# Optimization experiments

Hardware: AMD Instinct MI355X
Metric: run time of the kernel (lower is better)

## Reference

```python
import jax, jax.numpy as jnp
import numpy as np

LSTM_SIZE = 64
NUM_OPS = 5
NUM_LAYERS = 7  # 2 warmup anchors + 5 sampled layers (layer_id 2..6)


def _lstm_cell(x, h, c, w_ih, w_hh, b_ih, b_hh):
    # torch LSTMCell gate order: i, f, g, o
    g = x @ w_ih.T + b_ih + h @ w_hh.T + b_hh  # [1, 4*64]
    i, f, gg, o = jnp.split(g, 4, axis=1)
    c2 = jax.nn.sigmoid(f) * c + jax.nn.sigmoid(i) * jnp.tanh(gg)
    h2 = jax.nn.sigmoid(o) * jnp.tanh(c2)
    return h2, c2


def _sampler(embed, w_ih, w_hh, b_ih, b_hh, w_soft, b_soft, b_soft_no_learn,
             w_attn1, w_attn2, v_attn, prev_c, prev_h, use_bias, key):
    keys = jax.random.split(key, 20)  # 5 layers * (2 index + 2 op) samples
    k = 0
    anchors, anchors_w1, arc_seq = [], [], []
    log_prob = jnp.float32(0.0)
    entropy = jnp.float32(0.0)
    inputs = embed[0][None, :]
    # warmup: two anchor slots (anchors are zeros, per original code)
    for _ in range(2):
        prev_h, prev_c = _lstm_cell(inputs, prev_h, prev_c, w_ih, w_hh, b_ih, b_hh)
        anchors.append(jnp.zeros((1, LSTM_SIZE), jnp.float32))
        anchors_w1.append(prev_h @ w_attn1.T)
    for layer_id in range(2, NUM_LAYERS):
        idxs, ops = [], []
        # sample 2 previous-layer indices via tiny attention
        for _ in range(2):
            prev_h, prev_c = _lstm_cell(inputs, prev_h, prev_c, w_ih, w_hh, b_ih, b_hh)
            query = jnp.concatenate(anchors_w1, axis=0)            # [layer_id, 64]
            q = jnp.tanh(query + prev_h @ w_attn2.T)               # broadcast [layer_id, 64]
            logits = (q @ v_attn.T).reshape(layer_id)              # [layer_id]
            logits = logits / 5.0 + 1.1 * jnp.tanh(logits)
            index = jax.random.categorical(keys[k], logits); k += 1
            logp = jax.nn.log_softmax(logits)
            log_prob = log_prob + (-logp[index])
            entropy = entropy + jax.lax.stop_gradient(-jnp.sum(logp * jnp.exp(logp)))
            idxs.append(index)
            A = jnp.concatenate(anchors, axis=0)                   # [layer_id, 64]
            inputs = A[index][None, :]
        # sample 2 ops
        for _ in range(2):
            prev_h, prev_c = _lstm_cell(inputs, prev_h, prev_c, w_ih, w_hh, b_ih, b_hh)
            logits = (prev_h @ w_soft.T + b_soft)                  # [1, 5]
            logits = 1.1 / 2.5 * jnp.tanh(logits / 5.0)
            if use_bias:
                logits = logits + b_soft_no_learn
            logits = logits[0]
            op_id = jax.random.categorical(keys[k], logits); k += 1
            logp = jax.nn.log_softmax(logits)
            log_prob = log_prob + (-logp[op_id])
            entropy = entropy + jax.lax.stop_gradient(-jnp.sum(logp * jnp.exp(logp)))
            ops.append(op_id)
            inputs = embed[op_id + 1][None, :]
        # extra step producing this layer's anchor
        prev_h, prev_c = _lstm_cell(inputs, prev_h, prev_c, w_ih, w_hh, b_ih, b_hh)
        anchors.append(prev_h)
        anchors_w1.append(prev_h @ w_attn1.T)
        inputs = embed[0][None, :]
        # arc layout per layer after in-place fixups: [idx1, op1, idx2, op2]
        arc_seq += [idxs[0], ops[0], idxs[1], ops[1]]
    arc = jnp.stack(arc_seq)
    return arc, entropy, log_prob, prev_c, prev_h


def setup_inputs() -> dict:
    key = jax.random.key(0)
    ks = jax.random.split(key, 9)
    u = lambda k, shape: jax.random.uniform(k, shape, jnp.float32, -0.1, 0.1)
    return {
        "embed": u(ks[0], (6, LSTM_SIZE)),
        "w_ih": u(ks[1], (4 * LSTM_SIZE, LSTM_SIZE)),
        "w_hh": u(ks[2], (4 * LSTM_SIZE, LSTM_SIZE)),
        "b_ih": u(ks[3], (4 * LSTM_SIZE,)),
        "b_hh": u(ks[4], (4 * LSTM_SIZE,)),
        "w_soft": u(ks[5], (NUM_OPS, LSTM_SIZE)),
        "b_soft": jnp.array([[10.0, 10.0, 0.0, 0.0, 0.0]], jnp.float32),
        "b_soft_no_learn": jnp.array([[0.25, 0.25, -0.25, -0.25, -0.25]], jnp.float32),
        "w_attn1": u(ks[6], (LSTM_SIZE, LSTM_SIZE)),
        "w_attn2": u(ks[7], (LSTM_SIZE, LSTM_SIZE)),
        "v_attn": u(ks[8], (1, LSTM_SIZE)),
        "seed": 0,
    }


def reference(embed, w_ih, w_hh, b_ih, b_hh, w_soft, b_soft, b_soft_no_learn,
              w_attn1, w_attn2, v_attn, seed):
    key = jax.random.key(seed)
    k1, k2 = jax.random.split(key)
    zc = jnp.zeros((1, LSTM_SIZE), jnp.float32)
    zh = jnp.zeros((1, LSTM_SIZE), jnp.float32)
    arc1, ent1, lp1, c, h = _sampler(embed, w_ih, w_hh, b_ih, b_hh, w_soft, b_soft,
                                     b_soft_no_learn, w_attn1, w_attn2, v_attn,
                                     zc, zh, True, k1)
    arc2, ent2, lp2, _, _ = _sampler(embed, w_ih, w_hh, b_ih, b_hh, w_soft, b_soft,
                                     b_soft_no_learn, w_attn1, w_attn2, v_attn,
                                     c, h, False, k2)
    return (arc1, arc2, lp1 + lp2, ent1 + ent2)
```

## Files before the change

kernel.cpp:

```cpp
#include <hip/hip_runtime.h>
#include <cstdint>

#ifndef FASTMATH
#define FASTMATH 1
#endif

#define NT 512

__device__ __forceinline__ uint32_t rotl32_(uint32_t v, int d) {
  return (v << d) | (v >> (32 - d));
}

__device__ __forceinline__ void tf2x32(uint32_t k0, uint32_t k1,
                                       uint32_t x0, uint32_t x1,
                                       uint32_t& o0, uint32_t& o1) {
  const uint32_t k2 = k0 ^ k1 ^ 0x1BD11BDAu;
  x0 += k0; x1 += k1;
#define TF4(a,b,c,d) \
  x0 += x1; x1 = rotl32_(x1,a); x1 ^= x0; \
  x0 += x1; x1 = rotl32_(x1,b); x1 ^= x0; \
  x0 += x1; x1 = rotl32_(x1,c); x1 ^= x0; \
  x0 += x1; x1 = rotl32_(x1,d); x1 ^= x0;
  TF4(13,15,26,6)
  x0 += k1; x1 += k2 + 1u;
  TF4(17,29,16,24)
  x0 += k2; x1 += k0 + 2u;
  TF4(13,15,26,6)
  x0 += k0; x1 += k1 + 3u;
  TF4(17,29,16,24)
  x0 += k1; x1 += k2 + 4u;
  TF4(13,15,26,6)
  x0 += k2; x1 += k0 + 5u;
#undef TF4
  o0 = x0; o1 = x1;
}

#if FASTMATH
__device__ __forceinline__ float tanh_(float x) {
  float e = __expf(2.0f * x);
  return 1.0f - __fdividef(2.0f, e + 1.0f);
}
__device__ __forceinline__ float sig_(float x) {
  return __fdividef(1.0f, 1.0f + __expf(-x));
}
#define log_ __logf
#define exp_ __expf
#else
__device__ __forceinline__ float tanh_(float x) { return tanhf(x); }
__device__ __forceinline__ float sig_(float x) { return 0.5f * tanhf(0.5f * x) + 0.5f; }
#define log_ logf
#define exp_ expf
#endif

template <int CTRL>
__device__ __forceinline__ float dppf(float x) {
  return __int_as_float(__builtin_amdgcn_update_dpp(
      0, __float_as_int(x), CTRL, 0xF, 0xF, true));
}
template <int CTRL>
__device__ __forceinline__ int dppi(int x) {
  return __builtin_amdgcn_update_dpp(0, x, CTRL, 0xF, 0xF, true);
}
constexpr int QP1 = 0xB1;
constexpr int QP2 = 0x4E;
constexpr int HM  = 0x141;

__global__ __launch_bounds__(NT, 1)
void nas_controller(const float* __restrict__ embed,
                    const float* __restrict__ w_ih,
                    const float* __restrict__ w_hh,
                    const float* __restrict__ b_ih,
                    const float* __restrict__ b_hh,
                    const float* __restrict__ w_soft,
                    const float* __restrict__ b_soft,
                    const float* __restrict__ b_soft_nl,
                    const float* __restrict__ w_attn1,
                    const float* __restrict__ w_attn2,
                    const float* __restrict__ v_attn,
                    const int* __restrict__ seedp,
                    float* __restrict__ out) {
  const int tid  = threadIdx.x;
  const int lane = tid & 63;
  const int wid  = tid >> 6;
  const int row  = tid >> 1;
  const int half = tid & 1;

  __shared__ __align__(16) float attn1L[64 * 68];
  __shared__ __align__(16) float attn2L[64 * 68];
  __shared__ __align__(16) float wsoftL[5 * 68 + 8];
  __shared__ __align__(16) float vaL[64];
  __shared__ __align__(16) float preQ[13 * 256];
  __shared__ __align__(16) float aw1sL[8 * 68];
  __shared__ __align__(16) float hw2L[64];
  __shared__ __align__(16) float hB[64];
  __shared__ float cs[64];
  __shared__ float gates[256];
  __shared__ float gL[320];
  __shared__ float lSave[320];
  __shared__ float lpT[40], entT[40];
  __shared__ int   biSave[40];
  __shared__ float bsoftL[8], bnlL[8];
  __shared__ int   seliL;

  float4 wi[8], wh[8];
  {
    const float4* a = reinterpret_cast<const float4*>(w_ih) + row * 16 + half * 8;
#pragma unroll
    for (int j = 0; j < 8; ++j) wi[j] = a[j];
    const float4* b = reinterpret_cast<const float4*>(w_hh) + row * 16 + half * 8;
#pragma unroll
    for (int j = 0; j < 8; ++j) wh[j] = b[j];
  }
  const float bsum = b_ih[row] + b_hh[row];

  for (int i4 = tid; i4 < 1024; i4 += NT) {
    int r = i4 >> 4, c4 = i4 & 15;
    reinterpret_cast<float4*>(attn1L)[r * 17 + c4] =
        reinterpret_cast<const float4*>(w_attn1)[i4];
    reinterpret_cast<float4*>(attn2L)[r * 17 + c4] =
        reinterpret_cast<const float4*>(w_attn2)[i4];
  }
  for (int i = tid; i < 340; i += NT) {
    int r = i / 68, c = i % 68;
    wsoftL[i] = (c < 64) ? w_soft[r * 64 + c] : 0.f;
  }
  if (tid < 64) { vaL[tid] = v_attn[tid]; hB[tid] = 0.f; cs[tid] = 0.f; }
  if (tid < 8) {
    bsoftL[tid] = (tid < 5) ? b_soft[tid] : 0.f;
    bnlL[tid]   = (tid < 5) ? b_soft_nl[tid] : 0.f;
  }
  preQ[6 * 256 + tid] = 0.f;

  if (tid < 320) {
    int s_ = (tid >= 160) ? 1 : 0;
    int rem = tid - s_ * 160;
    int k = rem >> 3, i = rem & 7;
    uint32_t a, b, ka, kb, o0, o1;
    tf2x32(0u, (uint32_t)seedp[0], 0u, (uint32_t)s_, a, b);
    tf2x32(a, b, 0u, (uint32_t)k, ka, kb);
    tf2x32(ka, kb, 0u, (uint32_t)i, o0, o1);
    uint32_t bits = o0 ^ o1;
    const float TINY = 1.1754943508222875e-38f;
    float uu = __uint_as_float((bits >> 9) | 0x3f800000u) - 1.0f;
    uu = uu * (1.0f - TINY) + TINY;
    uu = fmaxf(TINY, uu);
    gL[tid] = -log_(-log_(uu));
  }

#pragma unroll
  for (int e = 0; e < 6; ++e) {
    const float4* x4 = reinterpret_cast<const float4*>(embed + e * 64) + half * 8;
    float a0 = 0, a1 = 0, a2 = 0, a3 = 0;
#pragma unroll
    for (int j = 0; j < 8; ++j) {
      float4 x = x4[j], w = wi[j];
      a0 = fmaf(w.x, x.x, a0); a1 = fmaf(w.y, x.y, a1);
      a2 = fmaf(w.z, x.z, a2); a3 = fmaf(w.w, x.w, a3);
    }
    float acc = (a0 + a1) + (a2 + a3);
    acc += __shfl_xor(acc, 1);
    if (half == 0) preQ[e * 256 + row] = acc;
  }

  __syncthreads();

  const float4* hU = reinterpret_cast<const float4*>(hB);
  float hacc = 0.f;
  int srcSlot = 0, sIdx = 0;

  auto nonlin = [&]() {
    if (tid < 64) {
      float gi = gates[tid], gf = gates[64 + tid];
      float gg = gates[128 + tid], go = gates[192 + tid];
      float c2 = sig_(gf) * cs[tid] + sig_(gi) * tanh_(gg);
      float h2 = sig_(go) * tanh_(c2);
      cs[tid] = c2; hB[tid] = h2;
    }
  };

  auto hdotAcc = [&]() -> float {
    const float4* h4 = reinterpret_cast<const float4*>(hB) + half * 8;
    float a0 = 0, a1 = 0, a2 = 0, a3 = 0;
#pragma unroll
    for (int j = 0; j < 8; ++j) {
      float4 x = h4[j], w = wh[j];
      a0 = fmaf(w.x, x.x, a0); a1 = fmaf(w.y, x.y, a1);
      a2 = fmaf(w.z, x.z, a2); a3 = fmaf(w.w, x.w, a3);
    }
    float acc = (a0 + a1) + (a2 + a3);
    acc += __shfl_xor(acc, 1);
    return acc;
  };

  auto matvecAll = [&](const float* W, float* dst) {
    const int r8 = tid >> 3, q = tid & 7;
    const float4* w4 = reinterpret_cast<const float4*>(W + r8 * 68 + q * 8);
    float4 wa = w4[0], wb = w4[1];
    const float4* h4 = reinterpret_cast<const float4*>(hB) + q * 2;
    float4 ha = h4[0], hb = h4[1];
    float acc = fmaf(wa.x, ha.x, fmaf(wa.y, ha.y, fmaf(wa.z, ha.z, wa.w * ha.w)));
    acc += fmaf(wb.x, hb.x, fmaf(wb.y, hb.y, fmaf(wb.z, hb.z, wb.w * hb.w)));
    acc += __shfl_xor(acc, 1);
    acc += __shfl_xor(acc, 2);
    acc += __shfl_xor(acc, 4);
    if (q == 0) dst[r8] = acc;
  };

  auto anchorPre = [&](int slot) {
    const float4* h4 = reinterpret_cast<const float4*>(hB) + half * 8;
    float a0 = 0, a1 = 0, a2 = 0, a3 = 0;
#pragma unroll
    for (int j = 0; j < 8; ++j) {
      float4 x = h4[j], w = wi[j];
      a0 = fmaf(w.x, x.x, a0); a1 = fmaf(w.y, x.y, a1);
      a2 = fmaf(w.z, x.z, a2); a3 = fmaf(w.w, x.w, a3);
    }
    float acc = (a0 + a1) + (a2 + a3);
    acc += __shfl_xor(acc, 1);
    if (half == 0) preQ[slot * 256 + row] = acc;
  };

  auto doSel = [&](int n, int k, int mode, float raw, float* op) {
    float l;
    if (lane < n) {
      if (mode == 0) l = raw / 5.0f + 1.1f * tanh_(raw);
      else {
        l = (float)(1.1 / 2.5) * tanh_(raw / 5.0f);
        if (mode == 1) l += bnlL[lane];
      }
    } else l = -INFINITY;
    if (lane < 8) lSave[(sIdx * 20 + k) * 8 + lane] = l;
    float g = (lane < n) ? gL[sIdx * 160 + k * 8 + lane] : 0.f;
    float v = (lane < n) ? (l + g) : -INFINITY;
    int bi = lane & 7;
#define ARGSTEP(C) { float ov = dppf<C>(v); int oi = dppi<C>(bi); \
    bool tk = (ov > v) || (ov == v && oi < bi); if (tk) { v = ov; bi = oi; } }
    ARGSTEP(QP1) ARGSTEP(QP2) ARGSTEP(HM)
#undef ARGSTEP
    if (lane == 0) {
      seliL = bi;
      biSave[sIdx * 20 + k] = bi;
      op[0] = (float)bi;
    }
  };

  for (int s = 0; s < 2; ++s) {
    sIdx = s;
    srcSlot = 0;
    for (int w = 0; w < 2; ++w) {
      if (half == 0) gates[row] = hacc + preQ[srcSlot * 256 + row] + bsum;
      __syncthreads();
      nonlin();
      __syncthreads();
      hacc = hdotAcc();
      matvecAll(attn1L, aw1sL + w * 68);
      __syncthreads();
    }
    int keyk = 0;
    for (int L = 2; L <= 6; ++L) {
      for (int t = 0; t < 2; ++t) {
        if (half == 0) gates[row] = hacc + preQ[srcSlot * 256 + row] + bsum;
        __syncthreads();
        nonlin();
        __syncthreads();
        hacc = hdotAcc();
        matvecAll(attn2L, hw2L);
        __syncthreads();
        if (wid == 0) {
          const int g8 = lane >> 3, j = lane & 7;
          float sacc = 0.f;
          if (g8 < L) {
            const float4* aw = reinterpret_cast<const float4*>(aw1sL + g8 * 68 + j * 8);
            const float4* hq = reinterpret_cast<const float4*>(hw2L + j * 8);
            const float4* vq = reinterpret_cast<const float4*>(vaL + j * 8);
            float4 A0 = aw[0], A1 = aw[1], H0 = hq[0], H1 = hq[1], V0 = vq[0], V1 = vq[1];
            sacc = fmaf(tanh_(A0.x + H0.x), V0.x, sacc);
            sacc = fmaf(tanh_(A0.y + H0.y), V0.y, sacc);
            sacc = fmaf(tanh_(A0.z + H0.z), V0.z, sacc);
            sacc = fmaf(tanh_(A0.w + H0.w), V0.w, sacc);
            sacc = fmaf(tanh_(A1.x + H1.x), V1.x, sacc);
            sacc = fmaf(tanh_(A1.y + H1.y), V1.y, sacc);
            sacc = fmaf(tanh_(A1.z + H1.z), V1.z, sacc);
            sacc = fmaf(tanh_(A1.w + H1.w), V1.w, sacc);
          }
          sacc += dppf<QP1>(sacc); sacc += dppf<QP2>(sacc); sacc += dppf<HM>(sacc);
          float raw = __shfl(sacc, lane << 3);
          doSel(L, keyk, 0, raw, out + s * 20 + (L - 2) * 4 + t * 2);
        }
        keyk++;
        __syncthreads();
        srcSlot = 6 + seliL;
      }
      for (int t = 0; t < 2; ++t) {
        if (half == 0) gates[row] = hacc + preQ[srcSlot * 256 + row] + bsum;
        __syncthreads();
        nonlin();
        __syncthreads();
        hacc = hdotAcc();
        if (wid == 0) {
          const int g8 = lane >> 3, j = lane & 7;
          float sacc = 0.f;
          if (g8 < 5) {
            const float4* wq = reinterpret_cast<const float4*>(wsoftL + g8 * 68 + j * 8);
            float4 wa = wq[0], wb = wq[1];
            float4 ha = hU[j * 2], hb = hU[j * 2 + 1];
            sacc = fmaf(wa.x, ha.x, fmaf(wa.y, ha.y, fmaf(wa.z, ha.z, wa.w * ha.w)));
            sacc += fmaf(wb.x, hb.x, fmaf(wb.y, hb.y, fmaf(wb.z, hb.z, wb.w * hb.w)));
          }
          sacc += dppf<QP1>(sacc); sacc += dppf<QP2>(sacc); sacc += dppf<HM>(sacc);
          float raw = __shfl(sacc, lane << 3) + bsoftL[lane & 7];
          doSel(5, keyk, (s == 0) ? 1 : 2, raw,
                out + s * 20 + (L - 2) * 4 + t * 2 + 1);
        }
        keyk++;
        __syncthreads();
        srcSlot = 1 + seliL;
      }
      if (half == 0) gates[row] = hacc + preQ[srcSlot * 256 + row] + bsum;
      __syncthreads();
      nonlin();
      __syncthreads();
      hacc = hdotAcc();
      matvecAll(attn1L, aw1sL + L * 68);
      anchorPre(6 + L);
      __syncthreads();
      srcSlot = 0;
    }
  }

  __syncthreads();
  if (tid < 320) {
    int j = tid >> 3, c = tid & 7;
    float l = lSave[j * 8 + c];
    float mx = l;
    mx = fmaxf(mx, dppf<QP1>(mx)); mx = fmaxf(mx, dppf<QP2>(mx)); mx = fmaxf(mx, dppf<HM>(mx));
    float e = (l == -INFINITY) ? 0.f : exp_(l - mx);
    float ss = e; ss += dppf<QP1>(ss); ss += dppf<QP2>(ss); ss += dppf<HM>(ss);
    float lse = log_(ss);
    float lpi = l - mx - lse;
    float ec = (l == -INFINITY) ? 0.f : lpi * exp_(lpi);
    ec += dppf<QP1>(ec); ec += dppf<QP2>(ec); ec += dppf<HM>(ec);
    if (c == 0) entT[j] = -ec;
    if (c == biSave[j]) lpT[j] = -(l - mx - lse);
  }
  __syncthreads();
  if (tid == 0) {
    float lp = 0.f, ent = 0.f;
    for (int j = 0; j < 40; ++j) { lp += lpT[j]; ent += entT[j]; }
    out[40] = lp; out[41] = ent;
  }
}

extern "C" void kernel_launch(void* const* d_in, const int* in_sizes, int n_in,
                              void* d_out, int out_size, void* d_ws, size_t ws_size,
                              hipStream_t stream) {
  (void)in_sizes; (void)n_in; (void)out_size; (void)d_ws; (void)ws_size;
  nas_controller<<<1, NT, 0, stream>>>(
      (const float*)d_in[0],
      (const float*)d_in[1],
      (const float*)d_in[2],
      (const float*)d_in[3],
      (const float*)d_in[4],
      (const float*)d_in[5],
      (const float*)d_in[6],
      (const float*)d_in[7],
      (const float*)d_in[8],
      (const float*)d_in[9],
      (const float*)d_in[10],
      (const int*)d_in[11],
      (float*)d_out);
}
```

Baseline: 72.72 us.

## Remap gate rows so each wave computes LSTM nonlinearity in registers, double-buffer h

Rows are remapped so that the four gates of each hidden unit sit in neighbouring lanes of one wave. The cell update then runs with shuffles and DPP in registers instead of going through a shared gates array and a separate 64-thread nonlinearity phase. The cell state stays in a register and h is double-buffered in shared memory, which removes one or two block barriers per LSTM step. This is aimed at the latency of this sequential chain, which is dominated by barriers. The cost is more transcendental work per thread and a subtle dependence on the parity toggle staying consistent across all paths.

```diff
diff --git a/kernel.cpp b/kernel.cpp
--- a/kernel.cpp
+++ b/kernel.cpp
@@ -82,8 +82,11 @@
   const int tid  = threadIdx.x;
   const int lane = tid & 63;
   const int wid  = tid >> 6;
-  const int row  = tid >> 1;
-  const int half = tid & 1;
+  const int unitl = lane >> 3;
+  const int gate  = (lane >> 1) & 3;
+  const int half  = lane & 1;
+  const int u     = wid * 8 + unitl;
+  const int row   = gate * 64 + u;
 
   __shared__ __align__(16) float attn1L[64 * 68];
   __shared__ __align__(16) float attn2L[64 * 68];
@@ -92,9 +95,7 @@
   __shared__ __align__(16) float preQ[13 * 256];
   __shared__ __align__(16) float aw1sL[8 * 68];
   __shared__ __align__(16) float hw2L[64];
-  __shared__ __align__(16) float hB[64];
-  __shared__ float cs[64];
-  __shared__ float gates[256];
+  __shared__ __align__(16) float hB[2][64];
   __shared__ float gL[320];
   __shared__ float lSave[320];
   __shared__ float lpT[40], entT[40];
@@ -124,7 +125,7 @@
     int r = i / 68, c = i % 68;
     wsoftL[i] = (c < 64) ? w_soft[r * 64 + c] : 0.f;
   }
-  if (tid < 64) { vaL[tid] = v_attn[tid]; hB[tid] = 0.f; cs[tid] = 0.f; }
+  if (tid < 64) { vaL[tid] = v_attn[tid]; hB[0][tid] = 0.f; hB[1][tid] = 0.f; }
   if (tid < 8) {
     bsoftL[tid] = (tid < 5) ? b_soft[tid] : 0.f;
     bnlL[tid]   = (tid < 5) ? b_soft_nl[tid] : 0.f;
@@ -164,22 +165,25 @@
 
   __syncthreads();
 
-  const float4* hU = reinterpret_cast<const float4*>(hB);
+  float creg = 0.f;
   float hacc = 0.f;
+  int par = 0;
   int srcSlot = 0, sIdx = 0;
 
-  auto nonlin = [&]() {
-    if (tid < 64) {
-      float gi = gates[tid], gf = gates[64 + tid];
-      float gg = gates[128 + tid], go = gates[192 + tid];
-      float c2 = sig_(gf) * cs[tid] + sig_(gi) * tanh_(gg);
-      float h2 = sig_(go) * tanh_(c2);
-      cs[tid] = c2; hB[tid] = h2;
-    }
+  auto nonlinStep = [&]() {
+    float gsum = hacc + preQ[srcSlot * 256 + row] + bsum;
+    float nl = (gate == 2) ? tanh_(gsum) : sig_(gsum);
+    float sw4 = __shfl_xor(nl, 4);
+    float P = (gate & 1) ? (((gate == 1) ? nl : sw4) * creg)
+                         : (nl * sw4);
+    float c2 = P + dppf<QP2>(P);
+    creg = c2;
+    if ((lane & 7) == 6) hB[par ^ 1][u] = nl * tanh_(c2);
+    par ^= 1;
   };
 
   auto hdotAcc = [&]() -> float {
-    const float4* h4 = reinterpret_cast<const float4*>(hB) + half * 8;
+    const float4* h4 = reinterpret_cast<const float4*>(hB[par]) + half * 8;
     float a0 = 0, a1 = 0, a2 = 0, a3 = 0;
 #pragma unroll
     for (int j = 0; j < 8; ++j) {
@@ -196,7 +200,7 @@
     const int r8 = tid >> 3, q = tid & 7;
     const float4* w4 = reinterpret_cast<const float4*>(W + r8 * 68 + q * 8);
     float4 wa = w4[0], wb = w4[1];
-    const float4* h4 = reinterpret_cast<const float4*>(hB) + q * 2;
+    const float4* h4 = reinterpret_cast<const float4*>(hB[par]) + q * 2;
     float4 ha = h4[0], hb = h4[1];
     float acc = fmaf(wa.x, ha.x, fmaf(wa.y, ha.y, fmaf(wa.z, ha.z, wa.w * ha.w)));
     acc += fmaf(wb.x, hb.x, fmaf(wb.y, hb.y, fmaf(wb.z, hb.z, wb.w * hb.w)));
@@ -207,7 +211,7 @@
   };
 
   auto anchorPre = [&](int slot) {
-    const float4* h4 = reinterpret_cast<const float4*>(hB) + half * 8;
+    const float4* h4 = reinterpret_cast<const float4*>(hB[par]) + half * 8;
     float a0 = 0, a1 = 0, a2 = 0, a3 = 0;
 #pragma unroll
     for (int j = 0; j < 8; ++j) {
@@ -248,23 +252,18 @@
     sIdx = s;
     srcSlot = 0;
     for (int w = 0; w < 2; ++w) {
-      if (half == 0) gates[row] = hacc + preQ[srcSlot * 256 + row] + bsum;
+      nonlinStep();
       __syncthreads();
-      nonlin();
-      __syncthreads();
+      matvecAll(attn1L, aw1sL + w * 68);
       hacc = hdotAcc();
-      matvecAll(attn1L, aw1sL + w * 68);
-      __syncthreads();
     }
     int keyk = 0;
     for (int L = 2; L <= 6; ++L) {
       for (int t = 0; t < 2; ++t) {
-        if (half == 0) gates[row] = hacc + preQ[srcSlot * 256 + row] + bsum;
-        __syncthreads();
-        nonlin();
-        __syncthreads();
+        nonlinStep();
+        __syncthreads();
+        matvecAll(attn2L, hw2L);
         hacc = hdotAcc();
-        matvecAll(attn2L, hw2L);
         __syncthreads();
         if (wid == 0) {
           const int g8 = lane >> 3, j = lane & 7;
@@ -292,9 +291,7 @@
         srcSlot = 6 + seliL;
       }
       for (int t = 0; t < 2; ++t) {
-        if (half == 0) gates[row] = hacc + preQ[srcSlot * 256 + row] + bsum;
-        __syncthreads();
-        nonlin();
+        nonlinStep();
         __syncthreads();
         hacc = hdotAcc();
         if (wid == 0) {
@@ -303,7 +300,8 @@
           if (g8 < 5) {
             const float4* wq = reinterpret_cast<const float4*>(wsoftL + g8 * 68 + j * 8);
             float4 wa = wq[0], wb = wq[1];
-            float4 ha = hU[j * 2], hb = hU[j * 2 + 1];
+            const float4* h4 = reinterpret_cast<const float4*>(hB[par]) + j * 2;
+            float4 ha = h4[0], hb = h4[1];
             sacc = fmaf(wa.x, ha.x, fmaf(wa.y, ha.y, fmaf(wa.z, ha.z, wa.w * ha.w)));
             sacc += fmaf(wb.x, hb.x, fmaf(wb.y, hb.y, fmaf(wb.z, hb.z, wb.w * hb.w)));
           }
@@ -316,14 +314,11 @@
         __syncthreads();
         srcSlot = 1 + seliL;
       }
-      if (half == 0) gates[row] = hacc + preQ[srcSlot * 256 + row] + bsum;
+      nonlinStep();
       __syncthreads();
-      nonlin();
-      __syncthreads();
-      hacc = hdotAcc();
       matvecAll(attn1L, aw1sL + L * 68);
       anchorPre(6 + L);
-      __syncthreads();
+      hacc = hdotAcc();
       srcSlot = 0;
     }
   }
```

Result: slower. 75.27 us (+3.5%).
